# Performance work log

Hardware: AMD Instinct MI355X
Metric: run time of the kernel (lower is better)

The kernel has to match this reference:

```python
import jax, jax.numpy as jnp
import numpy as np

INPUT_SZ = 16
HPF = 32  # hidden_per_feat_sz
INTERACTIONS = [(0, 1), (2, 3), (4, 5), (6, 7)]
N_INT = len(INTERACTIONS)
INPUT_SIZE = INPUT_SZ + 2 * N_INT          # 24
HIDDEN = (INPUT_SZ + N_INT) * HPF          # 640
BATCH, SEQ = 128, 512

# static masks, faithful to the torch code (note: only even-indexed interactions
# get U_mask rows, exactly as the original loop `range(0, len(interactions), 2)`)
_Um = np.zeros((INPUT_SIZE, HIDDEN), np.float32)
for i in range(INPUT_SZ):
    _Um[i, i * HPF:(i + 1) * HPF] = 1
for i in range(0, N_INT, 2):
    _Um[i + INPUT_SZ, i * HPF:(i + 1) * HPF] = 1
    _Um[i + INPUT_SZ + 1, i * HPF:(i + 1) * HPF] = 1
U_MASK = jnp.asarray(_Um)
V_MASK = jnp.asarray(np.kron(np.eye(INPUT_SZ + N_INT, dtype=np.float32),
                             np.ones((HPF, HPF), np.float32)))
FEAT_SEQ = np.array(list(range(INPUT_SZ)) + [f for p in INTERACTIONS for f in p])


def setup_inputs() -> dict:
    key = jax.random.key(0)
    ks = jax.random.split(key, 13)
    stdv = 1.0 / np.sqrt(HIDDEN)
    u = lambda k, s: jax.random.uniform(k, s, jnp.float32, -stdv, stdv)
    inp = {"x": jax.random.normal(ks[0], (BATCH, SEQ, INPUT_SZ), jnp.float32)}
    names = ["i", "f", "c", "o"]
    for j, n in enumerate(names):
        inp[f"U_{n}"] = u(ks[1 + 3 * j], (INPUT_SIZE, HIDDEN))
        inp[f"V_{n}"] = u(ks[2 + 3 * j], (HIDDEN, HIDDEN))
        inp[f"b_{n}"] = u(ks[3 + 3 * j], (HIDDEN,))
    return inp


def reference(x, U_i, V_i, b_i, U_f, V_f, b_f, U_c, V_c, b_c, U_o, V_o, b_o):
    # gather masked-feature view of inputs once: [B, T, INPUT_SIZE]
    xg = x[:, :, FEAT_SEQ]
    # precompute masked, gate-concatenated weights (i|f|c|o)
    Ucat = jnp.concatenate([U_i * U_MASK, U_f * U_MASK,
                            U_c * U_MASK, U_o * U_MASK], axis=1)   # [in, 4H]
    Vcat = jnp.concatenate([V_i * V_MASK, V_f * V_MASK,
                            V_c * V_MASK, V_o * V_MASK], axis=1)   # [H, 4H]
    bcat = jnp.concatenate([b_i, b_f, b_c, b_o])                   # [4H]
    # input contribution for all timesteps in one GEMM: [B, T, 4H]
    xU = jnp.einsum('bti,ig->btg', xg, Ucat) + bcat

    h0 = jnp.zeros((x.shape[0], HIDDEN), x.dtype)
    c0 = jnp.zeros_like(h0)

    def step(carry, xu_t):
        h, c = carry
        gates = xu_t + h @ Vcat
        i_t, f_t, g_t, o_t = jnp.split(gates, 4, axis=-1)
        c = jax.nn.sigmoid(f_t) * c + jax.nn.sigmoid(i_t) * jnp.tanh(g_t)
        h = jax.nn.sigmoid(o_t) * jnp.tanh(c)
        return (h, c), h

    (h_t, c_t), hs = jax.lax.scan(step, (h0, c0), jnp.swapaxes(xU, 0, 1))
    hidden_seq = jnp.swapaxes(hs, 0, 1)  # [B, T, H]
    return hidden_seq, (h_t, c_t)
```

## Files before the change

### kernel.cpp

```cpp
#include <hip/hip_runtime.h>


#define TT 512
#define HN 640
#define BN 128

typedef float f2 __attribute__((ext_vector_type(2)));
typedef unsigned int u32x4 __attribute__((ext_vector_type(4)));

__global__ __attribute__((amdgpu_flat_work_group_size(64, 64)))
void lstm_kernel(
    const float* __restrict__ x,
    const float* __restrict__ Ui, const float* __restrict__ Vi, const float* __restrict__ bi,
    const float* __restrict__ Uf, const float* __restrict__ Vf, const float* __restrict__ bf,
    const float* __restrict__ Uc, const float* __restrict__ Vc, const float* __restrict__ bc,
    const float* __restrict__ Uo, const float* __restrict__ Vo, const float* __restrict__ bo,
    float* __restrict__ out) {
  __shared__ __align__(16) float lds[4544];

  const int unit = blockIdx.x;
  const int lane = threadIdx.x;
  const int j  = unit >> 6;
  const int bp = unit & 63;
  const int gp = lane >> 5;
  const int n  = lane & 31;
  const int col = j * 32 + n;
  const int b  = bp * 2 + gp;

  const float LOG2E = 1.44269504088896340736f;
  const float Bs = -LOG2E;
  const float Bg = -2.f * LOG2E;

  if (lane < 32) {
    for (int k = 0; k < 32; ++k) {
      const int r = (j * 32 + k) * HN + col;
      lds[n * 132 + k * 4 + 0] = Bs * Vi[r];
      lds[n * 132 + k * 4 + 1] = Bs * Vf[r];
      lds[n * 132 + k * 4 + 2] = Bg * Vc[r];
      lds[n * 132 + k * 4 + 3] = Bs * Vo[r];
    }
  }

  int f1 = 0, f2i = 0;
  if (j < 16) { f1 = f2i = j; if (j == 0) f2i = 1; else if (j == 2) f2i = 3; }
  auto uw = [&](const float* __restrict__ U, float& w1, float& w2) {
    w1 = 0.f; w2 = 0.f;
    if (j < 16) {
      w1 = U[j * HN + col];
      if (j == 0)      { w1 += U[16 * HN + col]; w2 = U[17 * HN + col]; }
      else if (j == 2) { w1 += U[18 * HN + col]; w2 = U[19 * HN + col]; }
    }
  };
  float wi1, wi2, wf1, wf2, wg1, wg2, wo1, wo2;
  uw(Ui, wi1, wi2); uw(Uf, wf1, wf2); uw(Uc, wg1, wg2); uw(Uo, wo1, wo2);
  const f2 w11IF = {Bs * wi1, Bs * wf1}, w21IF = {Bs * wi2, Bs * wf2};
  const f2 w11GO = {Bg * wg1, Bs * wo1}, w21GO = {Bg * wg2, Bs * wo2};
  const f2 bsIF  = {Bs * bi[col], Bs * bf[col]};
  const f2 bsGO  = {Bg * bc[col], Bs * bo[col]};

  const unsigned zb    = (unsigned)(unsigned long long)&lds[0];
  const unsigned wrd   = zb + (unsigned)n * 528u;
  const unsigned laddr = zb + 16896u + (unsigned)lane * 4u;
  const unsigned hrd   = zb + 16896u + (unsigned)gp * 128u;
  const unsigned xw    = zb + 17152u + (unsigned)lane * 4u;
  const unsigned xrb   = zb + 17152u + (unsigned)gp * 512u;

  u32x4 xsrd, osrd;
  { const unsigned long long a = (unsigned long long)x;
    xsrd.x = (unsigned)a; xsrd.y = (unsigned)(a >> 32);
    xsrd.z = (unsigned)(BN * TT * 16 * 4); xsrd.w = 0x00020000u; }
  { const unsigned long long a = (unsigned long long)out;
    osrd.x = (unsigned)a; osrd.y = (unsigned)(a >> 32);
    osrd.z = (unsigned)((BN * TT * HN + 2 * BN * HN) * 4); osrd.w = 0x00020000u; }

  unsigned voff  = (unsigned)((b * TT * HN + col) * 4);
  unsigned xvoff = (unsigned)((((bp * 2) * TT + lane) * 16 + f1) * 4);
  const int sfd  = (f2i - f1) * 4;

  float h = 0.f, c = 0.f;

  asm volatile(
    "s_waitcnt lgkmcnt(0)\n\t"
    "ds_read_b128 v[96:99],   %[wrd]\n\t"
    "ds_read_b128 v[100:103], %[wrd] offset:16\n\t"
    "ds_read_b128 v[104:107], %[wrd] offset:32\n\t"
    "ds_read_b128 v[108:111], %[wrd] offset:48\n\t"
    "ds_read_b128 v[112:115], %[wrd] offset:64\n\t"
    "ds_read_b128 v[116:119], %[wrd] offset:80\n\t"
    "ds_read_b128 v[120:123], %[wrd] offset:96\n\t"
    "ds_read_b128 v[124:127], %[wrd] offset:112\n\t"
    "ds_read_b128 v[128:131], %[wrd] offset:128\n\t"
    "ds_read_b128 v[132:135], %[wrd] offset:144\n\t"
    "ds_read_b128 v[136:139], %[wrd] offset:160\n\t"
    "ds_read_b128 v[140:143], %[wrd] offset:176\n\t"
    "ds_read_b128 v[144:147], %[wrd] offset:192\n\t"
    "ds_read_b128 v[148:151], %[wrd] offset:208\n\t"
    "ds_read_b128 v[152:155], %[wrd] offset:224\n\t"
    "ds_read_b128 v[156:159], %[wrd] offset:240\n\t"
    "ds_read_b128 v[160:163], %[wrd] offset:256\n\t"
    "ds_read_b128 v[164:167], %[wrd] offset:272\n\t"
    "ds_read_b128 v[168:171], %[wrd] offset:288\n\t"
    "ds_read_b128 v[172:175], %[wrd] offset:304\n\t"
    "ds_read_b128 v[176:179], %[wrd] offset:320\n\t"
    "ds_read_b128 v[180:183], %[wrd] offset:336\n\t"
    "ds_read_b128 v[184:187], %[wrd] offset:352\n\t"
    "ds_read_b128 v[188:191], %[wrd] offset:368\n\t"
    "ds_read_b128 v[192:195], %[wrd] offset:384\n\t"
    "ds_read_b128 v[196:199], %[wrd] offset:400\n\t"
    "ds_read_b128 v[200:203], %[wrd] offset:416\n\t"
    "ds_read_b128 v[204:207], %[wrd] offset:432\n\t"
    "ds_read_b128 v[208:211], %[wrd] offset:448\n\t"
    "ds_read_b128 v[212:215], %[wrd] offset:464\n\t"
    "ds_read_b128 v[216:219], %[wrd] offset:480\n\t"
    "ds_read_b128 v[220:223], %[wrd] offset:496\n\t"
    "s_mov_b32 s22, 0x8000\n\t"
    "s_add_u32 s23, s22, %[sfd]\n\t"
    "buffer_load_dword v36, %[xvoff], %[xsrd], 0 offen\n\t"
    "buffer_load_dword v37, %[xvoff], %[xsrd], %[sfd] offen\n\t"
    "buffer_load_dword v38, %[xvoff], %[xsrd], s22 offen\n\t"
    "buffer_load_dword v39, %[xvoff], %[xsrd], s23 offen\n\t"
    "s_mov_b32 s21, 8\n\t"
    "Lchunk%=:\n\t"
    "s_waitcnt vmcnt(0)\n\t"
    "ds_write_b32 %[xw], v36\n\t"
    "ds_write_b32 %[xw], v37 offset:256\n\t"
    "ds_write_b32 %[xw], v38 offset:512\n\t"
    "ds_write_b32 %[xw], v39 offset:768\n\t"
    "v_add_u32 %[xvoff], 0x1000, %[xvoff]\n\t"
    "buffer_load_dword v36, %[xvoff], %[xsrd], 0 offen\n\t"
    "buffer_load_dword v37, %[xvoff], %[xsrd], %[sfd] offen\n\t"
    "buffer_load_dword v38, %[xvoff], %[xsrd], s22 offen\n\t"
    "buffer_load_dword v39, %[xvoff], %[xsrd], s23 offen\n\t"
    "v_mov_b32 v33, %[xrb]\n\t"
    "s_mov_b32 s20, 64\n\t"
    "Lstep%=:\n\t"
    "ds_write_b32 %[laddr], %[h]\n\t"
    "ds_read2_b32 v[88:89], v33 offset0:0 offset1:64\n\t"
    "ds_read_b128 v[48:51], %[hrd]\n\t"
    "ds_read_b128 v[52:55], %[hrd] offset:16\n\t"
    "ds_read_b128 v[56:59], %[hrd] offset:32\n\t"
    "ds_read_b128 v[60:63], %[hrd] offset:48\n\t"
    "ds_read_b128 v[64:67], %[hrd] offset:64\n\t"
    "ds_read_b128 v[68:71], %[hrd] offset:80\n\t"
    "ds_read_b128 v[72:75], %[hrd] offset:96\n\t"
    "ds_read_b128 v[76:79], %[hrd] offset:112\n\t"
    "v_add_u32 v33, 4, v33\n\t"
    "s_waitcnt lgkmcnt(8)\n\t"
    "v_pk_fma_f32 v[40:41], v[88:89], %[w11IF], %[bsIF] op_sel:[0,0,0] op_sel_hi:[0,1,1]\n\t"
    "v_pk_fma_f32 v[44:45], v[88:89], %[w11GO], %[bsGO] op_sel:[0,0,0] op_sel_hi:[0,1,1]\n\t"
    "v_pk_fma_f32 v[40:41], v[88:89], %[w21IF], v[40:41] op_sel:[1,0,0] op_sel_hi:[1,1,1]\n\t"
    "v_pk_fma_f32 v[44:45], v[88:89], %[w21GO], v[44:45] op_sel:[1,0,0] op_sel_hi:[1,1,1]\n\t"
    "v_mov_b32 v42, 0\n\t"
    "v_mov_b32 v43, 0\n\t"
    "v_mov_b32 v46, 0\n\t"
    "v_mov_b32 v47, 0\n\t"
    "s_waitcnt lgkmcnt(0)\n\t"
    "v_pk_fma_f32 v[40:41], v[96:97],   v[48:49], v[40:41] op_sel:[0,0,0] op_sel_hi:[1,0,1]\n\t"
    "v_pk_fma_f32 v[44:45], v[98:99],   v[48:49], v[44:45] op_sel:[0,0,0] op_sel_hi:[1,0,1]\n\t"
    "v_pk_fma_f32 v[42:43], v[100:101], v[48:49], v[42:43] op_sel:[0,1,0] op_sel_hi:[1,1,1]\n\t"
    "v_pk_fma_f32 v[46:47], v[102:103], v[48:49], v[46:47] op_sel:[0,1,0] op_sel_hi:[1,1,1]\n\t"
    "v_pk_fma_f32 v[40:41], v[104:105], v[50:51], v[40:41] op_sel:[0,0,0] op_sel_hi:[1,0,1]\n\t"
    "v_pk_fma_f32 v[44:45], v[106:107], v[50:51], v[44:45] op_sel:[0,0,0] op_sel_hi:[1,0,1]\n\t"
    "v_pk_fma_f32 v[42:43], v[108:109], v[50:51], v[42:43] op_sel:[0,1,0] op_sel_hi:[1,1,1]\n\t"
    "v_pk_fma_f32 v[46:47], v[110:111], v[50:51], v[46:47] op_sel:[0,1,0] op_sel_hi:[1,1,1]\n\t"
    "v_pk_fma_f32 v[40:41], v[112:113], v[52:53], v[40:41] op_sel:[0,0,0] op_sel_hi:[1,0,1]\n\t"
    "v_pk_fma_f32 v[44:45], v[114:115], v[52:53], v[44:45] op_sel:[0,0,0] op_sel_hi:[1,0,1]\n\t"
    "v_pk_fma_f32 v[42:43], v[116:117], v[52:53], v[42:43] op_sel:[0,1,0] op_sel_hi:[1,1,1]\n\t"
    "v_pk_fma_f32 v[46:47], v[118:119], v[52:53], v[46:47] op_sel:[0,1,0] op_sel_hi:[1,1,1]\n\t"
    "v_pk_fma_f32 v[40:41], v[120:121], v[54:55], v[40:41] op_sel:[0,0,0] op_sel_hi:[1,0,1]\n\t"
    "v_pk_fma_f32 v[44:45], v[122:123], v[54:55], v[44:45] op_sel:[0,0,0] op_sel_hi:[1,0,1]\n\t"
    "v_pk_fma_f32 v[42:43], v[124:125], v[54:55], v[42:43] op_sel:[0,1,0] op_sel_hi:[1,1,1]\n\t"
    "v_pk_fma_f32 v[46:47], v[126:127], v[54:55], v[46:47] op_sel:[0,1,0] op_sel_hi:[1,1,1]\n\t"
    "v_pk_fma_f32 v[40:41], v[128:129], v[56:57], v[40:41] op_sel:[0,0,0] op_sel_hi:[1,0,1]\n\t"
    "v_pk_fma_f32 v[44:45], v[130:131], v[56:57], v[44:45] op_sel:[0,0,0] op_sel_hi:[1,0,1]\n\t"
    "v_pk_fma_f32 v[42:43], v[132:133], v[56:57], v[42:43] op_sel:[0,1,0] op_sel_hi:[1,1,1]\n\t"
    "v_pk_fma_f32 v[46:47], v[134:135], v[56:57], v[46:47] op_sel:[0,1,0] op_sel_hi:[1,1,1]\n\t"
    "v_pk_fma_f32 v[40:41], v[136:137], v[58:59], v[40:41] op_sel:[0,0,0] op_sel_hi:[1,0,1]\n\t"
    "v_pk_fma_f32 v[44:45], v[138:139], v[58:59], v[44:45] op_sel:[0,0,0] op_sel_hi:[1,0,1]\n\t"
    "v_pk_fma_f32 v[42:43], v[140:141], v[58:59], v[42:43] op_sel:[0,1,0] op_sel_hi:[1,1,1]\n\t"
    "v_pk_fma_f32 v[46:47], v[142:143], v[58:59], v[46:47] op_sel:[0,1,0] op_sel_hi:[1,1,1]\n\t"
    "v_pk_fma_f32 v[40:41], v[144:145], v[60:61], v[40:41] op_sel:[0,0,0] op_sel_hi:[1,0,1]\n\t"
    "v_pk_fma_f32 v[44:45], v[146:147], v[60:61], v[44:45] op_sel:[0,0,0] op_sel_hi:[1,0,1]\n\t"
    "v_pk_fma_f32 v[42:43], v[148:149], v[60:61], v[42:43] op_sel:[0,1,0] op_sel_hi:[1,1,1]\n\t"
    "v_pk_fma_f32 v[46:47], v[150:151], v[60:61], v[46:47] op_sel:[0,1,0] op_sel_hi:[1,1,1]\n\t"
    "v_pk_fma_f32 v[40:41], v[152:153], v[62:63], v[40:41] op_sel:[0,0,0] op_sel_hi:[1,0,1]\n\t"
    "v_pk_fma_f32 v[44:45], v[154:155], v[62:63], v[44:45] op_sel:[0,0,0] op_sel_hi:[1,0,1]\n\t"
    "v_pk_fma_f32 v[42:43], v[156:157], v[62:63], v[42:43] op_sel:[0,1,0] op_sel_hi:[1,1,1]\n\t"
    "v_pk_fma_f32 v[46:47], v[158:159], v[62:63], v[46:47] op_sel:[0,1,0] op_sel_hi:[1,1,1]\n\t"
    "v_pk_fma_f32 v[40:41], v[160:161], v[64:65], v[40:41] op_sel:[0,0,0] op_sel_hi:[1,0,1]\n\t"
    "v_pk_fma_f32 v[44:45], v[162:163], v[64:65], v[44:45] op_sel:[0,0,0] op_sel_hi:[1,0,1]\n\t"
    "v_pk_fma_f32 v[42:43], v[164:165], v[64:65], v[42:43] op_sel:[0,1,0] op_sel_hi:[1,1,1]\n\t"
    "v_pk_fma_f32 v[46:47], v[166:167], v[64:65], v[46:47] op_sel:[0,1,0] op_sel_hi:[1,1,1]\n\t"
    "v_pk_fma_f32 v[40:41], v[168:169], v[66:67], v[40:41] op_sel:[0,0,0] op_sel_hi:[1,0,1]\n\t"
    "v_pk_fma_f32 v[44:45], v[170:171], v[66:67], v[44:45] op_sel:[0,0,0] op_sel_hi:[1,0,1]\n\t"
    "v_pk_fma_f32 v[42:43], v[172:173], v[66:67], v[42:43] op_sel:[0,1,0] op_sel_hi:[1,1,1]\n\t"
    "v_pk_fma_f32 v[46:47], v[174:175], v[66:67], v[46:47] op_sel:[0,1,0] op_sel_hi:[1,1,1]\n\t"
    "v_pk_fma_f32 v[40:41], v[176:177], v[68:69], v[40:41] op_sel:[0,0,0] op_sel_hi:[1,0,1]\n\t"
    "v_pk_fma_f32 v[44:45], v[178:179], v[68:69], v[44:45] op_sel:[0,0,0] op_sel_hi:[1,0,1]\n\t"
    "v_pk_fma_f32 v[42:43], v[180:181], v[68:69], v[42:43] op_sel:[0,1,0] op_sel_hi:[1,1,1]\n\t"
    "v_pk_fma_f32 v[46:47], v[182:183], v[68:69], v[46:47] op_sel:[0,1,0] op_sel_hi:[1,1,1]\n\t"
    "v_pk_fma_f32 v[40:41], v[184:185], v[70:71], v[40:41] op_sel:[0,0,0] op_sel_hi:[1,0,1]\n\t"
    "v_pk_fma_f32 v[44:45], v[186:187], v[70:71], v[44:45] op_sel:[0,0,0] op_sel_hi:[1,0,1]\n\t"
    "v_pk_fma_f32 v[42:43], v[188:189], v[70:71], v[42:43] op_sel:[0,1,0] op_sel_hi:[1,1,1]\n\t"
    "v_pk_fma_f32 v[46:47], v[190:191], v[70:71], v[46:47] op_sel:[0,1,0] op_sel_hi:[1,1,1]\n\t"
    "v_pk_fma_f32 v[40:41], v[192:193], v[72:73], v[40:41] op_sel:[0,0,0] op_sel_hi:[1,0,1]\n\t"
    "v_pk_fma_f32 v[44:45], v[194:195], v[72:73], v[44:45] op_sel:[0,0,0] op_sel_hi:[1,0,1]\n\t"
    "v_pk_fma_f32 v[42:43], v[196:197], v[72:73], v[42:43] op_sel:[0,1,0] op_sel_hi:[1,1,1]\n\t"
    "v_pk_fma_f32 v[46:47], v[198:199], v[72:73], v[46:47] op_sel:[0,1,0] op_sel_hi:[1,1,1]\n\t"
    "v_pk_fma_f32 v[40:41], v[200:201], v[74:75], v[40:41] op_sel:[0,0,0] op_sel_hi:[1,0,1]\n\t"
    "v_pk_fma_f32 v[44:45], v[202:203], v[74:75], v[44:45] op_sel:[0,0,0] op_sel_hi:[1,0,1]\n\t"
    "v_pk_fma_f32 v[42:43], v[204:205], v[74:75], v[42:43] op_sel:[0,1,0] op_sel_hi:[1,1,1]\n\t"
    "v_pk_fma_f32 v[46:47], v[206:207], v[74:75], v[46:47] op_sel:[0,1,0] op_sel_hi:[1,1,1]\n\t"
    "v_pk_fma_f32 v[40:41], v[208:209], v[76:77], v[40:41] op_sel:[0,0,0] op_sel_hi:[1,0,1]\n\t"
    "v_pk_fma_f32 v[44:45], v[210:211], v[76:77], v[44:45] op_sel:[0,0,0] op_sel_hi:[1,0,1]\n\t"
    "v_pk_fma_f32 v[42:43], v[212:213], v[76:77], v[42:43] op_sel:[0,1,0] op_sel_hi:[1,1,1]\n\t"
    "v_pk_fma_f32 v[46:47], v[214:215], v[76:77], v[46:47] op_sel:[0,1,0] op_sel_hi:[1,1,1]\n\t"
    "v_pk_fma_f32 v[40:41], v[216:217], v[78:79], v[40:41] op_sel:[0,0,0] op_sel_hi:[1,0,1]\n\t"
    "v_pk_fma_f32 v[44:45], v[218:219], v[78:79], v[44:45] op_sel:[0,0,0] op_sel_hi:[1,0,1]\n\t"
    "v_pk_fma_f32 v[42:43], v[220:221], v[78:79], v[42:43] op_sel:[0,1,0] op_sel_hi:[1,1,1]\n\t"
    "v_pk_fma_f32 v[46:47], v[222:223], v[78:79], v[46:47] op_sel:[0,1,0] op_sel_hi:[1,1,1]\n\t"
    "v_pk_add_f32 v[40:41], v[40:41], v[42:43]\n\t"
    "v_pk_add_f32 v[44:45], v[44:45], v[46:47]\n\t"
    "v_exp_f32 v80, v40\n\t"
    "v_exp_f32 v81, v41\n\t"
    "v_exp_f32 v82, v44\n\t"
    "v_exp_f32 v83, v45\n\t"
    "v_add_f32 v80, 1.0, v80\n\t"
    "v_add_f32 v81, 1.0, v81\n\t"
    "v_add_f32 v82, 1.0, v82\n\t"
    "v_add_f32 v83, 1.0, v83\n\t"
    "v_rcp_f32 v80, v80\n\t"
    "v_rcp_f32 v81, v81\n\t"
    "v_rcp_f32 v82, v82\n\t"
    "v_rcp_f32 v83, v83\n\t"
    "v_fma_f32 v82, 2.0, v82, -1.0\n\t"
    "v_mul_f32 v84, v80, v82\n\t"
    "v_fma_f32 %[c], v81, %[c], v84\n\t"
    "v_mul_f32 v85, 0xc038aa3b, %[c]\n\t"
    "v_exp_f32 v85, v85\n\t"
    "s_nop 1\n\t"
    "v_add_f32 v85, 1.0, v85\n\t"
    "v_rcp_f32 v85, v85\n\t"
    "s_nop 1\n\t"
    "v_fma_f32 v85, 2.0, v85, -1.0\n\t"
    "v_mul_f32 %[h], v83, v85\n\t"
    "buffer_store_dword %[h], %[voff], %[osrd], 0 offen\n\t"
    "v_add_u32 %[voff], 0xa00, %[voff]\n\t"
    "s_sub_u32 s20, s20, 1\n\t"
    "s_cmp_lg_u32 s20, 0\n\t"
    "s_cbranch_scc1 Lstep%=\n\t"
    "s_sub_u32 s21, s21, 1\n\t"
    "s_cmp_lg_u32 s21, 0\n\t"
    "s_cbranch_scc1 Lchunk%=\n\t"
    : [h]"+v"(h), [c]"+v"(c), [voff]"+v"(voff), [xvoff]"+v"(xvoff)
    : [laddr]"v"(laddr), [hrd]"v"(hrd), [xw]"v"(xw), [xrb]"v"(xrb),
      [wrd]"v"(wrd),
      [w11IF]"v"(w11IF), [w21IF]"v"(w21IF), [bsIF]"v"(bsIF),
      [w11GO]"v"(w11GO), [w21GO]"v"(w21GO), [bsGO]"v"(bsGO),
      [xsrd]"s"(xsrd), [osrd]"s"(osrd), [sfd]"s"(sfd)
    : "memory", "scc", "s20", "s21", "s22", "s23",
      "v33","v36","v37","v38","v39",
      "v40","v41","v42","v43","v44","v45","v46","v47",
      "v48","v49","v50","v51","v52","v53","v54","v55",
      "v56","v57","v58","v59","v60","v61","v62","v63",
      "v64","v65","v66","v67","v68","v69","v70","v71",
      "v72","v73","v74","v75","v76","v77","v78","v79",
      "v80","v81","v82","v83","v84","v85","v88","v89",
      "v96","v97","v98","v99","v100","v101","v102","v103",
      "v104","v105","v106","v107","v108","v109","v110","v111",
      "v112","v113","v114","v115","v116","v117","v118","v119",
      "v120","v121","v122","v123","v124","v125","v126","v127",
      "v128","v129","v130","v131","v132","v133","v134","v135",
      "v136","v137","v138","v139","v140","v141","v142","v143",
      "v144","v145","v146","v147","v148","v149","v150","v151",
      "v152","v153","v154","v155","v156","v157","v158","v159",
      "v160","v161","v162","v163","v164","v165","v166","v167",
      "v168","v169","v170","v171","v172","v173","v174","v175",
      "v176","v177","v178","v179","v180","v181","v182","v183",
      "v184","v185","v186","v187","v188","v189","v190","v191",
      "v192","v193","v194","v195","v196","v197","v198","v199",
      "v200","v201","v202","v203","v204","v205","v206","v207",
      "v208","v209","v210","v211","v212","v213","v214","v215",
      "v216","v217","v218","v219","v220","v221","v222","v223");

  out[BN * TT * HN + b * HN + col] = h;
  out[BN * TT * HN + BN * HN + b * HN + col] = c;
}

extern "C" void kernel_launch(void* const* d_in, const int* in_sizes, int n_in,
                              void* d_out, int out_size, void* d_ws, size_t ws_size,
                              hipStream_t stream) {
  (void)in_sizes; (void)n_in; (void)d_ws; (void)ws_size; (void)out_size;
  const float* x  = (const float*)d_in[0];
  const float* Ui = (const float*)d_in[1];
  const float* Vi = (const float*)d_in[2];
  const float* bi = (const float*)d_in[3];
  const float* Uf = (const float*)d_in[4];
  const float* Vf = (const float*)d_in[5];
  const float* bf = (const float*)d_in[6];
  const float* Uc = (const float*)d_in[7];
  const float* Vc = (const float*)d_in[8];
  const float* bc = (const float*)d_in[9];
  const float* Uo = (const float*)d_in[10];
  const float* Vo = (const float*)d_in[11];
  const float* bo = (const float*)d_in[12];
  float* out = (float*)d_out;

  dim3 grid(1280);
  dim3 block(64);
  hipLaunchKernelGGL(lstm_kernel, grid, block, 0, stream,
                     x, Ui, Vi, bi, Uf, Vf, bf, Uc, Vc, bc, Uo, Vo, bo, out);
}
```

Before: 390.4 us.

## Exchange hidden state and inputs via ds_bpermute instead of LDS staging

Replaces the per-step LDS write/read round trip of the hidden state with ds_bpermute cross-lane exchanges issued in groups of four and interleaved with the packed FMAs. The x inputs are kept in registers per lane and broadcast with bpermute instead of being staged through LDS, with a 32-step chunk and a smaller prefetch. This targets LDS write-to-read latency on the recurrent critical path. The cost is 32 bpermute ops per step instead of 8 wide reads, which may increase LDS instruction throughput pressure.

```diff
diff --git a/kernel.cpp b/kernel.cpp
--- a/kernel.cpp
+++ b/kernel.cpp
@@ -16,7 +16,7 @@
     const float* __restrict__ Uc, const float* __restrict__ Vc, const float* __restrict__ bc,
     const float* __restrict__ Uo, const float* __restrict__ Vo, const float* __restrict__ bo,
     float* __restrict__ out) {
-  __shared__ __align__(16) float lds[4544];
+  __shared__ __align__(16) float lds[4224];
 
   const int unit = blockIdx.x;
   const int lane = threadIdx.x;
@@ -58,12 +58,9 @@
   const f2 bsIF  = {Bs * bi[col], Bs * bf[col]};
   const f2 bsGO  = {Bg * bc[col], Bs * bo[col]};
 
-  const unsigned zb    = (unsigned)(unsigned long long)&lds[0];
-  const unsigned wrd   = zb + (unsigned)n * 528u;
-  const unsigned laddr = zb + 16896u + (unsigned)lane * 4u;
-  const unsigned hrd   = zb + 16896u + (unsigned)gp * 128u;
-  const unsigned xw    = zb + 17152u + (unsigned)lane * 4u;
-  const unsigned xrb   = zb + 17152u + (unsigned)gp * 512u;
+  const unsigned zb  = (unsigned)(unsigned long long)&lds[0];
+  const unsigned wrd = zb + (unsigned)n * 528u;
+  const unsigned hbb = (unsigned)(lane & 32) * 4u;
 
   u32x4 xsrd, osrd;
   { const unsigned long long a = (unsigned long long)x;
@@ -74,7 +71,7 @@
     osrd.z = (unsigned)((BN * TT * HN + 2 * BN * HN) * 4); osrd.w = 0x00020000u; }
 
   unsigned voff  = (unsigned)((b * TT * HN + col) * 4);
-  unsigned xvoff = (unsigned)((((bp * 2) * TT + lane) * 16 + f1) * 4);
+  unsigned xvoff = (unsigned)(((b * TT + (lane & 31)) * 16 + f1) * 4);
   const int sfd  = (f2i - f1) * 4;
 
   float h = 0.f, c = 0.f;
@@ -113,37 +110,30 @@
     "ds_read_b128 v[212:215], %[wrd] offset:464\n\t"
     "ds_read_b128 v[216:219], %[wrd] offset:480\n\t"
     "ds_read_b128 v[220:223], %[wrd] offset:496\n\t"
-    "s_mov_b32 s22, 0x8000\n\t"
-    "s_add_u32 s23, s22, %[sfd]\n\t"
-    "buffer_load_dword v36, %[xvoff], %[xsrd], 0 offen\n\t"
-    "buffer_load_dword v37, %[xvoff], %[xsrd], %[sfd] offen\n\t"
-    "buffer_load_dword v38, %[xvoff], %[xsrd], s22 offen\n\t"
-    "buffer_load_dword v39, %[xvoff], %[xsrd], s23 offen\n\t"
-    "s_mov_b32 s21, 8\n\t"
+    "buffer_load_dword v38, %[xvoff], %[xsrd], 0 offen\n\t"
+    "buffer_load_dword v39, %[xvoff], %[xsrd], %[sfd] offen\n\t"
+    "s_waitcnt lgkmcnt(0)\n\t"
+    "s_mov_b32 s21, 16\n\t"
     "Lchunk%=:\n\t"
     "s_waitcnt vmcnt(0)\n\t"
-    "ds_write_b32 %[xw], v36\n\t"
-    "ds_write_b32 %[xw], v37 offset:256\n\t"
-    "ds_write_b32 %[xw], v38 offset:512\n\t"
-    "ds_write_b32 %[xw], v39 offset:768\n\t"
-    "v_add_u32 %[xvoff], 0x1000, %[xvoff]\n\t"
-    "buffer_load_dword v36, %[xvoff], %[xsrd], 0 offen\n\t"
-    "buffer_load_dword v37, %[xvoff], %[xsrd], %[sfd] offen\n\t"
-    "buffer_load_dword v38, %[xvoff], %[xsrd], s22 offen\n\t"
-    "buffer_load_dword v39, %[xvoff], %[xsrd], s23 offen\n\t"
-    "v_mov_b32 v33, %[xrb]\n\t"
-    "s_mov_b32 s20, 64\n\t"
+    "v_mov_b32 v36, v38\n\t"
+    "v_mov_b32 v37, v39\n\t"
+    "v_add_u32 %[xvoff], 0x800, %[xvoff]\n\t"
+    "buffer_load_dword v38, %[xvoff], %[xsrd], 0 offen\n\t"
+    "buffer_load_dword v39, %[xvoff], %[xsrd], %[sfd] offen\n\t"
+    "v_mov_b32 v33, %[hbb]\n\t"
+    "s_mov_b32 s20, 32\n\t"
     "Lstep%=:\n\t"
-    "ds_write_b32 %[laddr], %[h]\n\t"
-    "ds_read2_b32 v[88:89], v33 offset0:0 offset1:64\n\t"
-    "ds_read_b128 v[48:51], %[hrd]\n\t"
-    "ds_read_b128 v[52:55], %[hrd] offset:16\n\t"
-    "ds_read_b128 v[56:59], %[hrd] offset:32\n\t"
-    "ds_read_b128 v[60:63], %[hrd] offset:48\n\t"
-    "ds_read_b128 v[64:67], %[hrd] offset:64\n\t"
-    "ds_read_b128 v[68:71], %[hrd] offset:80\n\t"
-    "ds_read_b128 v[72:75], %[hrd] offset:96\n\t"
-    "ds_read_b128 v[76:79], %[hrd] offset:112\n\t"
+    "ds_bpermute_b32 v88, v33, v36\n\t"
+    "ds_bpermute_b32 v89, v33, v37\n\t"
+    "ds_bpermute_b32 v48, %[hbb], %[h] offset:0\n\t"
+    "ds_bpermute_b32 v50, %[hbb], %[h] offset:4\n\t"
+    "ds_bpermute_b32 v52, %[hbb], %[h] offset:8\n\t"
+    "ds_bpermute_b32 v54, %[hbb], %[h] offset:12\n\t"
+    "ds_bpermute_b32 v56, %[hbb], %[h] offset:16\n\t"
+    "ds_bpermute_b32 v58, %[hbb], %[h] offset:20\n\t"
+    "ds_bpermute_b32 v60, %[hbb], %[h] offset:24\n\t"
+    "ds_bpermute_b32 v62, %[hbb], %[h] offset:28\n\t"
     "v_add_u32 v33, 4, v33\n\t"
     "s_waitcnt lgkmcnt(8)\n\t"
     "v_pk_fma_f32 v[40:41], v[88:89], %[w11IF], %[bsIF] op_sel:[0,0,0] op_sel_hi:[0,1,1]\n\t"
@@ -154,71 +144,102 @@
     "v_mov_b32 v43, 0\n\t"
     "v_mov_b32 v46, 0\n\t"
     "v_mov_b32 v47, 0\n\t"
-    "s_waitcnt lgkmcnt(0)\n\t"
+    "s_waitcnt lgkmcnt(4)\n\t"
     "v_pk_fma_f32 v[40:41], v[96:97],   v[48:49], v[40:41] op_sel:[0,0,0] op_sel_hi:[1,0,1]\n\t"
     "v_pk_fma_f32 v[44:45], v[98:99],   v[48:49], v[44:45] op_sel:[0,0,0] op_sel_hi:[1,0,1]\n\t"
-    "v_pk_fma_f32 v[42:43], v[100:101], v[48:49], v[42:43] op_sel:[0,1,0] op_sel_hi:[1,1,1]\n\t"
-    "v_pk_fma_f32 v[46:47], v[102:103], v[48:49], v[46:47] op_sel:[0,1,0] op_sel_hi:[1,1,1]\n\t"
-    "v_pk_fma_f32 v[40:41], v[104:105], v[50:51], v[40:41] op_sel:[0,0,0] op_sel_hi:[1,0,1]\n\t"
-    "v_pk_fma_f32 v[44:45], v[106:107], v[50:51], v[44:45] op_sel:[0,0,0] op_sel_hi:[1,0,1]\n\t"
-    "v_pk_fma_f32 v[42:43], v[108:109], v[50:51], v[42:43] op_sel:[0,1,0] op_sel_hi:[1,1,1]\n\t"
-    "v_pk_fma_f32 v[46:47], v[110:111], v[50:51], v[46:47] op_sel:[0,1,0] op_sel_hi:[1,1,1]\n\t"
-    "v_pk_fma_f32 v[40:41], v[112:113], v[52:53], v[40:41] op_sel:[0,0,0] op_sel_hi:[1,0,1]\n\t"
-    "v_pk_fma_f32 v[44:45], v[114:115], v[52:53], v[44:45] op_sel:[0,0,0] op_sel_hi:[1,0,1]\n\t"
-    "v_pk_fma_f32 v[42:43], v[116:117], v[52:53], v[42:43] op_sel:[0,1,0] op_sel_hi:[1,1,1]\n\t"
-    "v_pk_fma_f32 v[46:47], v[118:119], v[52:53], v[46:47] op_sel:[0,1,0] op_sel_hi:[1,1,1]\n\t"
-    "v_pk_fma_f32 v[40:41], v[120:121], v[54:55], v[40:41] op_sel:[0,0,0] op_sel_hi:[1,0,1]\n\t"
-    "v_pk_fma_f32 v[44:45], v[122:123], v[54:55], v[44:45] op_sel:[0,0,0] op_sel_hi:[1,0,1]\n\t"
-    "v_pk_fma_f32 v[42:43], v[124:125], v[54:55], v[42:43] op_sel:[0,1,0] op_sel_hi:[1,1,1]\n\t"
-    "v_pk_fma_f32 v[46:47], v[126:127], v[54:55], v[46:47] op_sel:[0,1,0] op_sel_hi:[1,1,1]\n\t"
-    "v_pk_fma_f32 v[40:41], v[128:129], v[56:57], v[40:41] op_sel:[0,0,0] op_sel_hi:[1,0,1]\n\t"
-    "v_pk_fma_f32 v[44:45], v[130:131], v[56:57], v[44:45] op_sel:[0,0,0] op_sel_hi:[1,0,1]\n\t"
-    "v_pk_fma_f32 v[42:43], v[132:133], v[56:57], v[42:43] op_sel:[0,1,0] op_sel_hi:[1,1,1]\n\t"
-    "v_pk_fma_f32 v[46:47], v[134:135], v[56:57], v[46:47] op_sel:[0,1,0] op_sel_hi:[1,1,1]\n\t"
-    "v_pk_fma_f32 v[40:41], v[136:137], v[58:59], v[40:41] op_sel:[0,0,0] op_sel_hi:[1,0,1]\n\t"
-    "v_pk_fma_f32 v[44:45], v[138:139], v[58:59], v[44:45] op_sel:[0,0,0] op_sel_hi:[1,0,1]\n\t"
-    "v_pk_fma_f32 v[42:43], v[140:141], v[58:59], v[42:43] op_sel:[0,1,0] op_sel_hi:[1,1,1]\n\t"
-    "v_pk_fma_f32 v[46:47], v[142:143], v[58:59], v[46:47] op_sel:[0,1,0] op_sel_hi:[1,1,1]\n\t"
-    "v_pk_fma_f32 v[40:41], v[144:145], v[60:61], v[40:41] op_sel:[0,0,0] op_sel_hi:[1,0,1]\n\t"
-    "v_pk_fma_f32 v[44:45], v[146:147], v[60:61], v[44:45] op_sel:[0,0,0] op_sel_hi:[1,0,1]\n\t"
-    "v_pk_fma_f32 v[42:43], v[148:149], v[60:61], v[42:43] op_sel:[0,1,0] op_sel_hi:[1,1,1]\n\t"
-    "v_pk_fma_f32 v[46:47], v[150:151], v[60:61], v[46:47] op_sel:[0,1,0] op_sel_hi:[1,1,1]\n\t"
-    "v_pk_fma_f32 v[40:41], v[152:153], v[62:63], v[40:41] op_sel:[0,0,0] op_sel_hi:[1,0,1]\n\t"
-    "v_pk_fma_f32 v[44:45], v[154:155], v[62:63], v[44:45] op_sel:[0,0,0] op_sel_hi:[1,0,1]\n\t"
-    "v_pk_fma_f32 v[42:43], v[156:157], v[62:63], v[42:43] op_sel:[0,1,0] op_sel_hi:[1,1,1]\n\t"
-    "v_pk_fma_f32 v[46:47], v[158:159], v[62:63], v[46:47] op_sel:[0,1,0] op_sel_hi:[1,1,1]\n\t"
-    "v_pk_fma_f32 v[40:41], v[160:161], v[64:65], v[40:41] op_sel:[0,0,0] op_sel_hi:[1,0,1]\n\t"
-    "v_pk_fma_f32 v[44:45], v[162:163], v[64:65], v[44:45] op_sel:[0,0,0] op_sel_hi:[1,0,1]\n\t"
-    "v_pk_fma_f32 v[42:43], v[164:165], v[64:65], v[42:43] op_sel:[0,1,0] op_sel_hi:[1,1,1]\n\t"
-    "v_pk_fma_f32 v[46:47], v[166:167], v[64:65], v[46:47] op_sel:[0,1,0] op_sel_hi:[1,1,1]\n\t"
-    "v_pk_fma_f32 v[40:41], v[168:169], v[66:67], v[40:41] op_sel:[0,0,0] op_sel_hi:[1,0,1]\n\t"
-    "v_pk_fma_f32 v[44:45], v[170:171], v[66:67], v[44:45] op_sel:[0,0,0] op_sel_hi:[1,0,1]\n\t"
-    "v_pk_fma_f32 v[42:43], v[172:173], v[66:67], v[42:43] op_sel:[0,1,0] op_sel_hi:[1,1,1]\n\t"
-    "v_pk_fma_f32 v[46:47], v[174:175], v[66:67], v[46:47] op_sel:[0,1,0] op_sel_hi:[1,1,1]\n\t"
-    "v_pk_fma_f32 v[40:41], v[176:177], v[68:69], v[40:41] op_sel:[0,0,0] op_sel_hi:[1,0,1]\n\t"
-    "v_pk_fma_f32 v[44:45], v[178:179], v[68:69], v[44:45] op_sel:[0,0,0] op_sel_hi:[1,0,1]\n\t"
-    "v_pk_fma_f32 v[42:43], v[180:181], v[68:69], v[42:43] op_sel:[0,1,0] op_sel_hi:[1,1,1]\n\t"
-    "v_pk_fma_f32 v[46:47], v[182:183], v[68:69], v[46:47] op_sel:[0,1,0] op_sel_hi:[1,1,1]\n\t"
-    "v_pk_fma_f32 v[40:41], v[184:185], v[70:71], v[40:41] op_sel:[0,0,0] op_sel_hi:[1,0,1]\n\t"
-    "v_pk_fma_f32 v[44:45], v[186:187], v[70:71], v[44:45] op_sel:[0,0,0] op_sel_hi:[1,0,1]\n\t"
-    "v_pk_fma_f32 v[42:43], v[188:189], v[70:71], v[42:43] op_sel:[0,1,0] op_sel_hi:[1,1,1]\n\t"
-    "v_pk_fma_f32 v[46:47], v[190:191], v[70:71], v[46:47] op_sel:[0,1,0] op_sel_hi:[1,1,1]\n\t"
-    "v_pk_fma_f32 v[40:41], v[192:193], v[72:73], v[40:41] op_sel:[0,0,0] op_sel_hi:[1,0,1]\n\t"
-    "v_pk_fma_f32 v[44:45], v[194:195], v[72:73], v[44:45] op_sel:[0,0,0] op_sel_hi:[1,0,1]\n\t"
-    "v_pk_fma_f32 v[42:43], v[196:197], v[72:73], v[42:43] op_sel:[0,1,0] op_sel_hi:[1,1,1]\n\t"
-    "v_pk_fma_f32 v[46:47], v[198:199], v[72:73], v[46:47] op_sel:[0,1,0] op_sel_hi:[1,1,1]\n\t"
-    "v_pk_fma_f32 v[40:41], v[200:201], v[74:75], v[40:41] op_sel:[0,0,0] op_sel_hi:[1,0,1]\n\t"
-    "v_pk_fma_f32 v[44:45], v[202:203], v[74:75], v[44:45] op_sel:[0,0,0] op_sel_hi:[1,0,1]\n\t"
-    "v_pk_fma_f32 v[42:43], v[204:205], v[74:75], v[42:43] op_sel:[0,1,0] op_sel_hi:[1,1,1]\n\t"
-    "v_pk_fma_f32 v[46:47], v[206:207], v[74:75], v[46:47] op_sel:[0,1,0] op_sel_hi:[1,1,1]\n\t"
-    "v_pk_fma_f32 v[40:41], v[208:209], v[76:77], v[40:41] op_sel:[0,0,0] op_sel_hi:[1,0,1]\n\t"
-    "v_pk_fma_f32 v[44:45], v[210:211], v[76:77], v[44:45] op_sel:[0,0,0] op_sel_hi:[1,0,1]\n\t"
-    "v_pk_fma_f32 v[42:43], v[212:213], v[76:77], v[42:43] op_sel:[0,1,0] op_sel_hi:[1,1,1]\n\t"
-    "v_pk_fma_f32 v[46:47], v[214:215], v[76:77], v[46:47] op_sel:[0,1,0] op_sel_hi:[1,1,1]\n\t"
-    "v_pk_fma_f32 v[40:41], v[216:217], v[78:79], v[40:41] op_sel:[0,0,0] op_sel_hi:[1,0,1]\n\t"
-    "v_pk_fma_f32 v[44:45], v[218:219], v[78:79], v[44:45] op_sel:[0,0,0] op_sel_hi:[1,0,1]\n\t"
-    "v_pk_fma_f32 v[42:43], v[220:221], v[78:79], v[42:43] op_sel:[0,1,0] op_sel_hi:[1,1,1]\n\t"
-    "v_pk_fma_f32 v[46:47], v[222:223], v[78:79], v[46:47] op_sel:[0,1,0] op_sel_hi:[1,1,1]\n\t"
+    "v_pk_fma_f32 v[42:43], v[100:101], v[50:51], v[42:43] op_sel:[0,0,0] op_sel_hi:[1,0,1]\n\t"
+    "v_pk_fma_f32 v[46:47], v[102:103], v[50:51], v[46:47] op_sel:[0,0,0] op_sel_hi:[1,0,1]\n\t"
+    "v_pk_fma_f32 v[40:41], v[104:105], v[52:53], v[40:41] op_sel:[0,0,0] op_sel_hi:[1,0,1]\n\t"
+    "v_pk_fma_f32 v[44:45], v[106:107], v[52:53], v[44:45] op_sel:[0,0,0] op_sel_hi:[1,0,1]\n\t"
+    "v_pk_fma_f32 v[42:43], v[108:109], v[54:55], v[42:43] op_sel:[0,0,0] op_sel_hi:[1,0,1]\n\t"
+    "v_pk_fma_f32 v[46:47], v[110:111], v[54:55], v[46:47] op_sel:[0,0,0] op_sel_hi:[1,0,1]\n\t"
+    "ds_bpermute_b32 v48, %[hbb], %[h] offset:32\n\t"
+    "ds_bpermute_b32 v50, %[hbb], %[h] offset:36\n\t"
+    "ds_bpermute_b32 v52, %[hbb], %[h] offset:40\n\t"
+    "ds_bpermute_b32 v54, %[hbb], %[h] offset:44\n\t"
+    "s_waitcnt lgkmcnt(4)\n\t"
+    "v_pk_fma_f32 v[40:41], v[112:113], v[56:57], v[40:41] op_sel:[0,0,0] op_sel_hi:[1,0,1]\n\t"
+    "v_pk_fma_f32 v[44:45], v[114:115], v[56:57], v[44:45] op_sel:[0,0,0] op_sel_hi:[1,0,1]\n\t"
+    "v_pk_fma_f32 v[42:43], v[116:117], v[58:59], v[42:43] op_sel:[0,0,0] op_sel_hi:[1,0,1]\n\t"
+    "v_pk_fma_f32 v[46:47], v[118:119], v[58:59], v[46:47] op_sel:[0,0,0] op_sel_hi:[1,0,1]\n\t"
+    "v_pk_fma_f32 v[40:41], v[120:121], v[60:61], v[40:41] op_sel:[0,0,0] op_sel_hi:[1,0,1]\n\t"
+    "v_pk_fma_f32 v[44:45], v[122:123], v[60:61], v[44:45] op_sel:[0,0,0] op_sel_hi:[1,0,1]\n\t"
+    "v_pk_fma_f32 v[42:43], v[124:125], v[62:63], v[42:43] op_sel:[0,0,0] op_sel_hi:[1,0,1]\n\t"
+    "v_pk_fma_f32 v[46:47], v[126:127], v[62:63], v[46:47] op_sel:[0,0,0] op_sel_hi:[1,0,1]\n\t"
+    "ds_bpermute_b32 v56, %[hbb], %[h] offset:48\n\t"
+    "ds_bpermute_b32 v58, %[hbb], %[h] offset:52\n\t"
+    "ds_bpermute_b32 v60, %[hbb], %[h] offset:56\n\t"
+    "ds_bpermute_b32 v62, %[hbb], %[h] offset:60\n\t"
+    "s_waitcnt lgkmcnt(4)\n\t"
+    "v_pk_fma_f32 v[40:41], v[128:129], v[48:49], v[40:41] op_sel:[0,0,0] op_sel_hi:[1,0,1]\n\t"
+    "v_pk_fma_f32 v[44:45], v[130:131], v[48:49], v[44:45] op_sel:[0,0,0] op_sel_hi:[1,0,1]\n\t"
+    "v_pk_fma_f32 v[42:43], v[132:133], v[50:51], v[42:43] op_sel:[0,0,0] op_sel_hi:[1,0,1]\n\t"
+    "v_pk_fma_f32 v[46:47], v[134:135], v[50:51], v[46:47] op_sel:[0,0,0] op_sel_hi:[1,0,1]\n\t"
+    "v_pk_fma_f32 v[40:41], v[136:137], v[52:53], v[40:41] op_sel:[0,0,0] op_sel_hi:[1,0,1]\n\t"
+    "v_pk_fma_f32 v[44:45], v[138:139], v[52:53], v[44:45] op_sel:[0,0,0] op_sel_hi:[1,0,1]\n\t"
+    "v_pk_fma_f32 v[42:43], v[140:141], v[54:55], v[42:43] op_sel:[0,0,0] op_sel_hi:[1,0,1]\n\t"
+    "v_pk_fma_f32 v[46:47], v[142:143], v[54:55], v[46:47] op_sel:[0,0,0] op_sel_hi:[1,0,1]\n\t"
+    "ds_bpermute_b32 v48, %[hbb], %[h] offset:64\n\t"
+    "ds_bpermute_b32 v50, %[hbb], %[h] offset:68\n\t"
+    "ds_bpermute_b32 v52, %[hbb], %[h] offset:72\n\t"
+    "ds_bpermute_b32 v54, %[hbb], %[h] offset:76\n\t"
+    "s_waitcnt lgkmcnt(4)\n\t"
+    "v_pk_fma_f32 v[40:41], v[144:145], v[56:57], v[40:41] op_sel:[0,0,0] op_sel_hi:[1,0,1]\n\t"
+    "v_pk_fma_f32 v[44:45], v[146:147], v[56:57], v[44:45] op_sel:[0,0,0] op_sel_hi:[1,0,1]\n\t"
+    "v_pk_fma_f32 v[42:43], v[148:149], v[58:59], v[42:43] op_sel:[0,0,0] op_sel_hi:[1,0,1]\n\t"
+    "v_pk_fma_f32 v[46:47], v[150:151], v[58:59], v[46:47] op_sel:[0,0,0] op_sel_hi:[1,0,1]\n\t"
+    "v_pk_fma_f32 v[40:41], v[152:153], v[60:61], v[40:41] op_sel:[0,0,0] op_sel_hi:[1,0,1]\n\t"
+    "v_pk_fma_f32 v[44:45], v[154:155], v[60:61], v[44:45] op_sel:[0,0,0] op_sel_hi:[1,0,1]\n\t"
+    "v_pk_fma_f32 v[42:43], v[156:157], v[62:63], v[42:43] op_sel:[0,0,0] op_sel_hi:[1,0,1]\n\t"
+    "v_pk_fma_f32 v[46:47], v[158:159], v[62:63], v[46:47] op_sel:[0,0,0] op_sel_hi:[1,0,1]\n\t"
+    "ds_bpermute_b32 v56, %[hbb], %[h] offset:80\n\t"
+    "ds_bpermute_b32 v58, %[hbb], %[h] offset:84\n\t"
+    "ds_bpermute_b32 v60, %[hbb], %[h] offset:88\n\t"
+    "ds_bpermute_b32 v62, %[hbb], %[h] offset:92\n\t"
+    "s_waitcnt lgkmcnt(4)\n\t"
+    "v_pk_fma_f32 v[40:41], v[160:161], v[48:49], v[40:41] op_sel:[0,0,0] op_sel_hi:[1,0,1]\n\t"
+    "v_pk_fma_f32 v[44:45], v[162:163], v[48:49], v[44:45] op_sel:[0,0,0] op_sel_hi:[1,0,1]\n\t"
+    "v_pk_fma_f32 v[42:43], v[164:165], v[50:51], v[42:43] op_sel:[0,0,0] op_sel_hi:[1,0,1]\n\t"
+    "v_pk_fma_f32 v[46:47], v[166:167], v[50:51], v[46:47] op_sel:[0,0,0] op_sel_hi:[1,0,1]\n\t"
+    "v_pk_fma_f32 v[40:41], v[168:169], v[52:53], v[40:41] op_sel:[0,0,0] op_sel_hi:[1,0,1]\n\t"
+    "v_pk_fma_f32 v[44:45], v[170:171], v[52:53], v[44:45] op_sel:[0,0,0] op_sel_hi:[1,0,1]\n\t"
+    "v_pk_fma_f32 v[42:43], v[172:173], v[54:55], v[42:43] op_sel:[0,0,0] op_sel_hi:[1,0,1]\n\t"
+    "v_pk_fma_f32 v[46:47], v[174:175], v[54:55], v[46:47] op_sel:[0,0,0] op_sel_hi:[1,0,1]\n\t"
+    "ds_bpermute_b32 v48, %[hbb], %[h] offset:96\n\t"
+    "ds_bpermute_b32 v50, %[hbb], %[h] offset:100\n\t"
+    "ds_bpermute_b32 v52, %[hbb], %[h] offset:104\n\t"
+    "ds_bpermute_b32 v54, %[hbb], %[h] offset:108\n\t"
+    "s_waitcnt lgkmcnt(4)\n\t"
+    "v_pk_fma_f32 v[40:41], v[176:177], v[56:57], v[40:41] op_sel:[0,0,0] op_sel_hi:[1,0,1]\n\t"
+    "v_pk_fma_f32 v[44:45], v[178:179], v[56:57], v[44:45] op_sel:[0,0,0] op_sel_hi:[1,0,1]\n\t"
+    "v_pk_fma_f32 v[42:43], v[180:181], v[58:59], v[42:43] op_sel:[0,0,0] op_sel_hi:[1,0,1]\n\t"
+    "v_pk_fma_f32 v[46:47], v[182:183], v[58:59], v[46:47] op_sel:[0,0,0] op_sel_hi:[1,0,1]\n\t"
+    "v_pk_fma_f32 v[40:41], v[184:185], v[60:61], v[40:41] op_sel:[0,0,0] op_sel_hi:[1,0,1]\n\t"
+    "v_pk_fma_f32 v[44:45], v[186:187], v[60:61], v[44:45] op_sel:[0,0,0] op_sel_hi:[1,0,1]\n\t"
+    "v_pk_fma_f32 v[42:43], v[188:189], v[62:63], v[42:43] op_sel:[0,0,0] op_sel_hi:[1,0,1]\n\t"
+    "v_pk_fma_f32 v[46:47], v[190:191], v[62:63], v[46:47] op_sel:[0,0,0] op_sel_hi:[1,0,1]\n\t"
+    "ds_bpermute_b32 v56, %[hbb], %[h] offset:112\n\t"
+    "ds_bpermute_b32 v58, %[hbb], %[h] offset:116\n\t"
+    "ds_bpermute_b32 v60, %[hbb], %[h] offset:120\n\t"
+    "ds_bpermute_b32 v62, %[hbb], %[h] offset:124\n\t"
+    "s_waitcnt lgkmcnt(4)\n\t"
+    "v_pk_fma_f32 v[40:41], v[192:193], v[48:49], v[40:41] op_sel:[0,0,0] op_sel_hi:[1,0,1]\n\t"
+    "v_pk_fma_f32 v[44:45], v[194:195], v[48:49], v[44:45] op_sel:[0,0,0] op_sel_hi:[1,0,1]\n\t"
+    "v_pk_fma_f32 v[42:43], v[196:197], v[50:51], v[42:43] op_sel:[0,0,0] op_sel_hi:[1,0,1]\n\t"
+    "v_pk_fma_f32 v[46:47], v[198:199], v[50:51], v[46:47] op_sel:[0,0,0] op_sel_hi:[1,0,1]\n\t"
+    "v_pk_fma_f32 v[40:41], v[200:201], v[52:53], v[40:41] op_sel:[0,0,0] op_sel_hi:[1,0,1]\n\t"
+    "v_pk_fma_f32 v[44:45], v[202:203], v[52:53], v[44:45] op_sel:[0,0,0] op_sel_hi:[1,0,1]\n\t"
+    "v_pk_fma_f32 v[42:43], v[204:205], v[54:55], v[42:43] op_sel:[0,0,0] op_sel_hi:[1,0,1]\n\t"
+    "v_pk_fma_f32 v[46:47], v[206:207], v[54:55], v[46:47] op_sel:[0,0,0] op_sel_hi:[1,0,1]\n\t"
+    "s_waitcnt lgkmcnt(0)\n\t"
+    "v_pk_fma_f32 v[40:41], v[208:209], v[56:57], v[40:41] op_sel:[0,0,0] op_sel_hi:[1,0,1]\n\t"
+    "v_pk_fma_f32 v[44:45], v[210:211], v[56:57], v[44:45] op_sel:[0,0,0] op_sel_hi:[1,0,1]\n\t"
+    "v_pk_fma_f32 v[42:43], v[212:213], v[58:59], v[42:43] op_sel:[0,0,0] op_sel_hi:[1,0,1]\n\t"
+    "v_pk_fma_f32 v[46:47], v[214:215], v[58:59], v[46:47] op_sel:[0,0,0] op_sel_hi:[1,0,1]\n\t"
+    "v_pk_fma_f32 v[40:41], v[216:217], v[60:61], v[40:41] op_sel:[0,0,0] op_sel_hi:[1,0,1]\n\t"
+    "v_pk_fma_f32 v[44:45], v[218:219], v[60:61], v[44:45] op_sel:[0,0,0] op_sel_hi:[1,0,1]\n\t"
+    "v_pk_fma_f32 v[42:43], v[220:221], v[62:63], v[42:43] op_sel:[0,0,0] op_sel_hi:[1,0,1]\n\t"
+    "v_pk_fma_f32 v[46:47], v[222:223], v[62:63], v[46:47] op_sel:[0,0,0] op_sel_hi:[1,0,1]\n\t"
     "v_pk_add_f32 v[40:41], v[40:41], v[42:43]\n\t"
     "v_pk_add_f32 v[44:45], v[44:45], v[46:47]\n\t"
     "v_exp_f32 v80, v40\n\t"
@@ -253,18 +274,15 @@
     "s_cmp_lg_u32 s21, 0\n\t"
     "s_cbranch_scc1 Lchunk%=\n\t"
     : [h]"+v"(h), [c]"+v"(c), [voff]"+v"(voff), [xvoff]"+v"(xvoff)
-    : [laddr]"v"(laddr), [hrd]"v"(hrd), [xw]"v"(xw), [xrb]"v"(xrb),
-      [wrd]"v"(wrd),
+    : [hbb]"v"(hbb), [wrd]"v"(wrd),
       [w11IF]"v"(w11IF), [w21IF]"v"(w21IF), [bsIF]"v"(bsIF),
       [w11GO]"v"(w11GO), [w21GO]"v"(w21GO), [bsGO]"v"(bsGO),
       [xsrd]"s"(xsrd), [osrd]"s"(osrd), [sfd]"s"(sfd)
-    : "memory", "scc", "s20", "s21", "s22", "s23",
+    : "memory", "scc", "s20", "s21",
       "v33","v36","v37","v38","v39",
       "v40","v41","v42","v43","v44","v45","v46","v47",
       "v48","v49","v50","v51","v52","v53","v54","v55",
       "v56","v57","v58","v59","v60","v61","v62","v63",
-      "v64","v65","v66","v67","v68","v69","v70","v71",
-      "v72","v73","v74","v75","v76","v77","v78","v79",
       "v80","v81","v82","v83","v84","v85","v88","v89",
       "v96","v97","v98","v99","v100","v101","v102","v103",
       "v104","v105","v106","v107","v108","v109","v110","v111",
```

Result: slower. 491.3 us (+25.8%).
